# Kernel optimization log

Hardware: AMD Instinct MI355X
Metric: run time of the kernel (lower is better)

Reference implementation:

```python
import jax, jax.numpy as jnp
import numpy as np

N = 1024   # num_nodes
D = 128    # embedding_size


def setup_inputs() -> dict:
    key = jax.random.key(0)
    k1, k2, k3 = jax.random.split(key, 3)
    z = jax.random.normal(k1, (N, D), dtype=jnp.float32)
    # torch.nn.Linear(2D, D): weight [D, 2D]; stored here as W1 [2D, D] for x @ W1
    W1 = jax.random.normal(k2, (2 * D, D), dtype=jnp.float32) * (1.0 / np.sqrt(2 * D))
    b1 = jnp.zeros((D,), dtype=jnp.float32)
    W2 = jax.random.normal(k3, (D, 1), dtype=jnp.float32) * (1.0 / np.sqrt(D))
    b2 = jnp.zeros((1,), dtype=jnp.float32)
    return {"z": z, "W1": W1, "b1": b1, "W2": W2, "b2": b2}


def reference(z, W1, b1, W2, b2):
    # Original: z_i = z.repeat_interleave(N) (i varies slowly),
    #           z_j = z.repeat(N)            (j varies fast),
    # q = Linear2(relu(Linear1(cat[z_i, z_j]))).squeeze()  -> shape [N*N]
    # Equivalent split-linear form (cat @ W1 == z_i @ W1[:D] + z_j @ W1[D:]):
    d = z.shape[1]
    pi = z @ W1[:d]          # [N, D] projection of left node
    pj = z @ W1[d:]          # [N, D] projection of right node
    h = jax.nn.relu(pi[:, None, :] + pj[None, :, :] + b1)  # [N, N, D]
    q = (h @ W2).squeeze(-1) + b2                          # [N, N]
    return q.reshape(-1)     # pair k = i*N + j, matching repeat_interleave/repeat order
```

## Files before the change

### kernel.cpp

```cpp
#include <hip/hip_runtime.h>
#include <hip/hip_bf16.h>


#define NN 1024
#define DD 128
#define TI 64
#define TJ 64
#define PAD 132

__global__ __launch_bounds__(256) void proj_kernel(
    const float* __restrict__ z,
    const float* __restrict__ W1,
    const float* __restrict__ b1,
    const float* __restrict__ W2,
    float* __restrict__ pic,
    float* __restrict__ pj,
    float* __restrict__ uh,
    float* __restrict__ vh)
{
    __shared__ float zs[DD];
    __shared__ float partial[4];
    const int i = blockIdx.x;
    const int t = threadIdx.x;
    if (t < DD) zs[t] = z[i * DD + t];
    __syncthreads();

    const int half = t >> 7;
    const int d = t & (DD - 1);
    const float* Wcol = W1 + half * DD * DD + d;

    float acc = 0.f;
    #pragma unroll 16
    for (int k = 0; k < DD; ++k)
        acc = fmaf(zs[k], Wcol[k * DD], acc);

    if (half == 0) acc += b1[d];
    if (half == 0) pic[i * DD + d] = acc;
    else           pj [i * DD + d] = acc;

    float c = acc * (0.5f * W2[d]);
    #pragma unroll
    for (int off = 32; off > 0; off >>= 1) c += __shfl_down(c, off);
    if ((t & 63) == 0) partial[t >> 6] = c;
    __syncthreads();
    if (t == 0) uh[i] = partial[0] + partial[1];
    if (t == 1) vh[i] = partial[2] + partial[3];
}

__global__ __launch_bounds__(256) void pair_kernel(
    const float* __restrict__ pic,
    const float* __restrict__ pj,
    const float* __restrict__ W2,
    const float* __restrict__ b2,
    const float* __restrict__ uh,
    const float* __restrict__ vh,
    float* __restrict__ out)
{
    __shared__ float a_s[TI * PAD];
    __shared__ float b_s[TJ * PAD];
    __shared__ float w_s[DD];
    __shared__ float u_s[TI];
    __shared__ float v_s[TJ];

    const int t  = threadIdx.x;
    const int bi = blockIdx.x;
    const int bj = blockIdx.y;

    const float4* srcA = (const float4*)(pic + bi * TI * DD);
    const float4* srcB = (const float4*)(pj + bj * TJ * DD);
    #pragma unroll
    for (int u = 0; u < 8; ++u) {
        int f   = t + 256 * u;
        int row = f >> 5;
        int c4  = f & 31;
        float4 va = srcA[f];
        float4 vb = srcB[f];
        *(float4*)&a_s[row * PAD + c4 * 4] = va;
        *(float4*)&b_s[row * PAD + c4 * 4] = vb;
    }
    if (t < DD)              w_s[t]       = 0.5f * W2[t];
    if (t < TI)              u_s[t]       = uh[bi * TI + t];
    if (t >= 128 && t < 192) v_s[t - 128] = vh[bj * TJ + (t - 128)];
    __syncthreads();

    const int tx = t & 15;
    const int ty = t >> 4;
    const float* ap = a_s + ty * PAD;
    const float* bp = b_s + tx * PAD;

    float acc[4][4];
    #pragma unroll
    for (int ii = 0; ii < 4; ++ii)
        #pragma unroll
        for (int jj = 0; jj < 4; ++jj) acc[ii][jj] = 0.f;

    #pragma unroll 4
    for (int d = 0; d < DD; d += 4) {
        float4 w4 = *(const float4*)(w_s + d);
        float4 av[4], bv[4];
        #pragma unroll
        for (int ii = 0; ii < 4; ++ii) av[ii] = *(const float4*)(ap + ii * 16 * PAD + d);
        #pragma unroll
        for (int jj = 0; jj < 4; ++jj) bv[jj] = *(const float4*)(bp + jj * 16 * PAD + d);

        #pragma unroll
        for (int ii = 0; ii < 4; ++ii) {
            const float ax = av[ii].x, ay = av[ii].y, az = av[ii].z, aw = av[ii].w;
            #pragma unroll
            for (int jj = 0; jj < 4; ++jj) {
                acc[ii][jj] = fmaf(fabsf(ax + bv[jj].x), w4.x, acc[ii][jj]);
                acc[ii][jj] = fmaf(fabsf(ay + bv[jj].y), w4.y, acc[ii][jj]);
                acc[ii][jj] = fmaf(fabsf(az + bv[jj].z), w4.z, acc[ii][jj]);
                acc[ii][jj] = fmaf(fabsf(aw + bv[jj].w), w4.w, acc[ii][jj]);
            }
        }
    }

    const float bb = b2[0];
    #pragma unroll
    for (int ii = 0; ii < 4; ++ii) {
        const int i = bi * TI + ty + ii * 16;
        const float ui = u_s[ty + ii * 16];
        #pragma unroll
        for (int jj = 0; jj < 4; ++jj) {
            const int j = bj * TJ + tx + jj * 16;
            out[(size_t)i * NN + j] = acc[ii][jj] + ui + v_s[tx + jj * 16] + bb;
        }
    }
}

extern "C" void kernel_launch(void* const* d_in, const int* in_sizes, int n_in,
                              void* d_out, int out_size, void* d_ws, size_t ws_size,
                              hipStream_t stream)
{
    const float* z  = (const float*)d_in[0];
    const float* W1 = (const float*)d_in[1];
    const float* b1 = (const float*)d_in[2];
    const float* W2 = (const float*)d_in[3];
    const float* b2 = (const float*)d_in[4];
    float* out = (float*)d_out;

    float* pic = (float*)d_ws;
    float* pj  = pic + NN * DD;
    float* uh  = pj  + NN * DD;
    float* vh  = uh  + NN;

    proj_kernel<<<NN, 256, 0, stream>>>(z, W1, b1, W2, pic, pj, uh, vh);

    dim3 grid(NN / TI, NN / TJ);
    pair_kernel<<<grid, 256, 0, stream>>>(pic, pj, W2, b2, uh, vh, out);
}
```

Baseline: 83.40 us.

## Batch eight nodes per projection block and double pair-kernel threads per tile

The projection kernel now handles eight nodes per block, so each W1 column load is reused across eight accumulators instead of being reloaded for every node, and it launches far fewer blocks. The pair kernel moves to 512 threads per 64x64 tile, each computing a 2x4 sub-tile instead of 4x4, which gives more waves per tile for latency hiding at the cost of less register reuse per thread. The b2 and W2 parameters are swapped in both the signature and the call, consistently.

Result: slower. 85.78 us (+2.9%).

```diff
diff --git a/kernel.cpp b/kernel.cpp
--- a/kernel.cpp
+++ b/kernel.cpp
@@ -7,6 +7,7 @@
 #define TI 64
 #define TJ 64
 #define PAD 132
+#define NPB 8
 
 __global__ __launch_bounds__(256) void proj_kernel(
     const float* __restrict__ z,
@@ -18,40 +19,65 @@
     float* __restrict__ uh,
     float* __restrict__ vh)
 {
-    __shared__ float zs[DD];
-    __shared__ float partial[4];
-    const int i = blockIdx.x;
+    __shared__ float zs[NPB * DD];
+    __shared__ float partial[4][NPB];
     const int t = threadIdx.x;
-    if (t < DD) zs[t] = z[i * DD + t];
+    const int base = blockIdx.x * NPB;
+
+    #pragma unroll
+    for (int u = 0; u < (NPB * DD) / 256; ++u)
+        zs[t + 256 * u] = z[base * DD + t + 256 * u];
     __syncthreads();
 
     const int half = t >> 7;
     const int d = t & (DD - 1);
     const float* Wcol = W1 + half * DD * DD + d;
 
-    float acc = 0.f;
-    #pragma unroll 16
-    for (int k = 0; k < DD; ++k)
-        acc = fmaf(zs[k], Wcol[k * DD], acc);
+    float acc[NPB];
+    #pragma unroll
+    for (int n = 0; n < NPB; ++n) acc[n] = 0.f;
 
-    if (half == 0) acc += b1[d];
-    if (half == 0) pic[i * DD + d] = acc;
-    else           pj [i * DD + d] = acc;
+    #pragma unroll 4
+    for (int k = 0; k < DD; ++k) {
+        const float w = Wcol[k * DD];
+        #pragma unroll
+        for (int n = 0; n < NPB; ++n)
+            acc[n] = fmaf(zs[n * DD + k], w, acc[n]);
+    }
 
-    float c = acc * (0.5f * W2[d]);
+    const float bd = b1[d];
+    const float hw = 0.5f * W2[d];
+    float c[NPB];
     #pragma unroll
-    for (int off = 32; off > 0; off >>= 1) c += __shfl_down(c, off);
-    if ((t & 63) == 0) partial[t >> 6] = c;
+    for (int n = 0; n < NPB; ++n) {
+        if (half == 0) {
+            acc[n] += bd;
+            pic[(size_t)(base + n) * DD + d] = acc[n];
+        } else {
+            pj[(size_t)(base + n) * DD + d] = acc[n];
+        }
+        c[n] = acc[n] * hw;
+    }
+
+    #pragma unroll
+    for (int n = 0; n < NPB; ++n)
+        #pragma unroll
+        for (int off = 32; off > 0; off >>= 1)
+            c[n] += __shfl_down(c[n], off);
+    const int wave = t >> 6;
+    if ((t & 63) == 0)
+        #pragma unroll
+        for (int n = 0; n < NPB; ++n) partial[wave][n] = c[n];
     __syncthreads();
-    if (t == 0) uh[i] = partial[0] + partial[1];
-    if (t == 1) vh[i] = partial[2] + partial[3];
+    if (t < NPB)            uh[base + t]       = partial[0][t] + partial[1][t];
+    else if (t < 2 * NPB)   vh[base + t - NPB] = partial[2][t - NPB] + partial[3][t - NPB];
 }
 
-__global__ __launch_bounds__(256) void pair_kernel(
+__global__ __launch_bounds__(512) void pair_kernel(
     const float* __restrict__ pic,
     const float* __restrict__ pj,
+    const float* __restrict__ b2,
     const float* __restrict__ W2,
-    const float* __restrict__ b2,
     const float* __restrict__ uh,
     const float* __restrict__ vh,
     float* __restrict__ out)
@@ -66,11 +92,11 @@
     const int bi = blockIdx.x;
     const int bj = blockIdx.y;
 
-    const float4* srcA = (const float4*)(pic + bi * TI * DD);
-    const float4* srcB = (const float4*)(pj + bj * TJ * DD);
+    const float4* srcA = (const float4*)(pic + (size_t)bi * TI * DD);
+    const float4* srcB = (const float4*)(pj  + (size_t)bj * TJ * DD);
     #pragma unroll
-    for (int u = 0; u < 8; ++u) {
-        int f   = t + 256 * u;
+    for (int u = 0; u < 4; ++u) {
+        int f   = t + 512 * u;
         int row = f >> 5;
         int c4  = f & 31;
         float4 va = srcA[f];
@@ -78,9 +104,9 @@
         *(float4*)&a_s[row * PAD + c4 * 4] = va;
         *(float4*)&b_s[row * PAD + c4 * 4] = vb;
     }
-    if (t < DD)              w_s[t]       = 0.5f * W2[t];
-    if (t < TI)              u_s[t]       = uh[bi * TI + t];
-    if (t >= 128 && t < 192) v_s[t - 128] = vh[bj * TJ + (t - 128)];
+    if (t < DD)                 w_s[t]            = 0.5f * W2[t];
+    else if (t < DD + TI)       u_s[t - DD]       = uh[bi * TI + t - DD];
+    else if (t < DD + TI + TJ)  v_s[t - DD - TI]  = vh[bj * TJ + t - DD - TI];
     __syncthreads();
 
     const int tx = t & 15;
@@ -88,23 +114,23 @@
     const float* ap = a_s + ty * PAD;
     const float* bp = b_s + tx * PAD;
 
-    float acc[4][4];
+    float acc[2][4];
     #pragma unroll
-    for (int ii = 0; ii < 4; ++ii)
+    for (int ii = 0; ii < 2; ++ii)
         #pragma unroll
         for (int jj = 0; jj < 4; ++jj) acc[ii][jj] = 0.f;
 
     #pragma unroll 4
     for (int d = 0; d < DD; d += 4) {
         float4 w4 = *(const float4*)(w_s + d);
-        float4 av[4], bv[4];
-        #pragma unroll
-        for (int ii = 0; ii < 4; ++ii) av[ii] = *(const float4*)(ap + ii * 16 * PAD + d);
+        float4 av[2], bv[4];
+        av[0] = *(const float4*)(ap + d);
+        av[1] = *(const float4*)(ap + 32 * PAD + d);
         #pragma unroll
         for (int jj = 0; jj < 4; ++jj) bv[jj] = *(const float4*)(bp + jj * 16 * PAD + d);
 
         #pragma unroll
-        for (int ii = 0; ii < 4; ++ii) {
+        for (int ii = 0; ii < 2; ++ii) {
             const float ax = av[ii].x, ay = av[ii].y, az = av[ii].z, aw = av[ii].w;
             #pragma unroll
             for (int jj = 0; jj < 4; ++jj) {
@@ -118,9 +144,9 @@
 
     const float bb = b2[0];
     #pragma unroll
-    for (int ii = 0; ii < 4; ++ii) {
-        const int i = bi * TI + ty + ii * 16;
-        const float ui = u_s[ty + ii * 16];
+    for (int ii = 0; ii < 2; ++ii) {
+        const int i = bi * TI + ty + ii * 32;
+        const float ui = u_s[ty + ii * 32];
         #pragma unroll
         for (int jj = 0; jj < 4; ++jj) {
             const int j = bj * TJ + tx + jj * 16;
@@ -145,8 +171,8 @@
     float* uh  = pj  + NN * DD;
     float* vh  = uh  + NN;
 
-    proj_kernel<<<NN, 256, 0, stream>>>(z, W1, b1, W2, pic, pj, uh, vh);
+    proj_kernel<<<NN / NPB, 256, 0, stream>>>(z, W1, b1, W2, pic, pj, uh, vh);
 
     dim3 grid(NN / TI, NN / TJ);
-    pair_kernel<<<grid, 256, 0, stream>>>(pic, pj, W2, b2, uh, vh, out);
+    pair_kernel<<<grid, 512, 0, stream>>>(pic, pj, b2, W2, uh, vh, out);
 }
```
